# Kernel optimization log

Measured on AMD Instinct MI355X. Metric: run time of the kernel, lower is better.

The kernel has to match this reference:

```python
import math
import jax, jax.numpy as jnp
import numpy as np

CROP_H = 28  # self.height
OUT_HW = 224  # final F.interpolate size


def _thetas_and_widths(boxes_np, H, W):
    """Host-side replication of cv2.minAreaRect/getAffineTransform + param2theta.
    boxes_np: [N,1,4] int (x1,y1,x3,y3). Returns thetas [N,2,3] f32, widths [N] int."""
    thetas, widths = [], []
    for b in boxes_np:
        x1, y1, x3, y3 = [float(v) for v in b[0]]
        bw, bh = abs(x3 - x1), abs(y3 - y1)
        box_w, box_h = max(bw, bh), min(bw, bh)  # minAreaRect + swap so box_w >= box_h
        wb = min(math.ceil(CROP_H * box_w / box_h), W)
        # cv2.getAffineTransform: affine maps (x1,y1)->(0,0), (x3,y1)->(wb,0), (x1,y3)->(0,CROP_H)
        src = np.array([[x1, y1, 1.0], [x3, y1, 1.0], [x1, y3, 1.0]], dtype=np.float64)
        dst = np.array([[0.0, 0.0], [wb, 0.0], [0.0, CROP_H]], dtype=np.float64)
        P = np.linalg.solve(src, dst)           # src @ P = dst -> affine = P.T (2x3)
        A = np.vstack([P.T, [0.0, 0.0, 1.0]])   # homogeneous 3x3
        Ai = np.linalg.inv(A)                    # param2theta inverts the affine
        th = np.zeros((2, 3), dtype=np.float64)
        th[0, 0] = Ai[0, 0]
        th[0, 1] = Ai[0, 1] * H / W
        th[0, 2] = Ai[0, 2] * 2.0 / W + th[0, 0] + th[0, 1] - 1.0
        th[1, 0] = Ai[1, 0] * W / H
        th[1, 1] = Ai[1, 1]
        th[1, 2] = Ai[1, 2] * 2.0 / H + th[1, 0] + th[1, 1] - 1.0
        thetas.append(th)
        widths.append(wb)
    return np.stack(thetas).astype(np.float32), np.array(widths, dtype=np.int64)


def _interp_matrix(out_size, in_size):
    """Row-stochastic linear-interpolation matrix, bilinear align_corners=True."""
    pos = jnp.linspace(0.0, in_size - 1.0, out_size)
    i0 = jnp.clip(jnp.floor(pos), 0, in_size - 2).astype(jnp.int32)
    t = pos - i0.astype(pos.dtype)
    r = jnp.arange(out_size)
    M = jnp.zeros((out_size, in_size), jnp.float32)
    return M.at[r, i0].add(1.0 - t).at[r, i0 + 1].add(t)


def _forward(feature, boxes, num_boxes):
    C, H, W = feature.shape[1], feature.shape[2], feature.shape[3]
    boxes_np = np.asarray(boxes)
    thetas_np, widths = _thetas_and_widths(boxes_np, H, W)
    thetas = jnp.asarray(thetas_np)                              # [N,2,3]

    # F.affine_grid(theta, (N,C,H,W), align_corners=True)
    xs = jnp.linspace(-1.0, 1.0, W)
    ys = jnp.linspace(-1.0, 1.0, H)
    gx0, gy0 = jnp.meshgrid(xs, ys, indexing='xy')               # [H,W]
    base = jnp.stack([gx0, gy0, jnp.ones_like(gx0)], axis=-1)    # [H,W,3]
    grid = jnp.einsum('nij,hwj->nhwi', thetas, base)             # [N,H,W,2] (x,y)

    # F.grid_sample bilinear, padding_mode='zeros', align_corners=True
    feat0 = feature[0]                                           # [C,H,W]
    ix = (grid[..., 0] + 1.0) * (W - 1) * 0.5                    # [N,H,W]
    iy = (grid[..., 1] + 1.0) * (H - 1) * 0.5
    x0f, y0f = jnp.floor(ix), jnp.floor(iy)
    x0, y0 = x0f.astype(jnp.int32), y0f.astype(jnp.int32)
    wx, wy = ix - x0f, iy - y0f

    def g(xi, yi):
        valid = (xi >= 0) & (xi < W) & (yi >= 0) & (yi < H)
        v = feat0[:, jnp.clip(yi, 0, H - 1), jnp.clip(xi, 0, W - 1)]  # [C,N,H,W]
        return v * valid[None].astype(feat0.dtype)

    rot = (((1 - wx) * (1 - wy))[None] * g(x0, y0)
           + (wx * (1 - wy))[None] * g(x0 + 1, y0)
           + ((1 - wx) * wy)[None] * g(x0, y0 + 1)
           + (wx * wy)[None] * g(x0 + 1, y0 + 1))                 # [C,N,H,W]
    rot = jnp.transpose(rot, (1, 0, 2, 3))                        # [N,C,H,W]

    # crop [:, :, :28, :w_i] and zero-pad to max width (mask == crop+pad)
    maxw = int(widths.max())
    mask = (jnp.arange(maxw)[None, :] < jnp.asarray(widths)[:, None]).astype(rot.dtype)
    cropped = rot[:, :, :CROP_H, :maxw] * mask[:, None, None, :]  # [N,C,28,maxw]

    # sort by width descending (np.argsort then reversed, as in the original)
    order = np.argsort(widths)[::-1].copy()
    cropped = cropped[jnp.asarray(order)]

    # F.interpolate to (224,224), bilinear, align_corners=True (separable)
    My = _interp_matrix(OUT_HW, CROP_H)                           # [224,28]
    Mx = _interp_matrix(OUT_HW, maxw)                             # [224,maxw]
    return jnp.einsum('nchw,ph,qw->ncpq', cropped, My, Mx)


def setup_inputs() -> dict:
    key = jax.random.key(0)
    N, C, H, W = 32, 32, 256, 256
    feature = jax.random.normal(key, (1, C, H, W), dtype=jnp.float32)
    rng = np.random.default_rng(0)
    x1 = rng.integers(0, 170, N)
    y1 = rng.integers(0, 200, N)
    bw = rng.integers(20, 80, N)
    bh = rng.integers(8, 48, N)
    x3 = np.minimum(x1 + bw, W - 1)
    y3 = np.minimum(y1 + bh, H - 1)
    boxes = jnp.asarray(np.stack([x1, y1, x3, y3], axis=1)[:, None, :].astype(np.int64))
    return {"feature": feature, "boxes": boxes, "num_boxes": N}


def reference(feature, boxes, num_boxes):
    return _forward(feature, boxes, num_boxes)
```

## Files before the change

### kernel.cpp

```cpp
#include <hip/hip_runtime.h>

#define NBOX   32
#define NCH    32
#define IMG    256
#define CROPH  28
#define OUTHW  224
#define TSTR   257

__device__ __forceinline__ void xss_stage(long long* k, int* a,
                                          const int* p, int mask) {
  long long nk[8]; int na[8];
  for (int j = 0; j < 8; ++j) {
    long long kb = k[p[j]]; int ab = a[p[j]];
    long long mn = (kb < k[j]) ? kb : k[j];
    long long mx = (kb < k[j]) ? k[j] : kb;
    long long sel = ((mask >> j) & 1) ? mx : mn;
    na[j] = (sel == k[j]) ? a[j] : ab;
    nk[j] = sel;
  }
  for (int j = 0; j < 8; ++j) { k[j] = nk[j]; a[j] = na[j]; }
}
__device__ __forceinline__ void xss_rev(long long* k, int* a) {
  for (int j = 0; j < 4; ++j) {
    long long tk = k[j]; k[j] = k[7-j]; k[7-j] = tk;
    int ta = a[j]; a[j] = a[7-j]; a[7-j] = ta;
  }
}
__device__ __forceinline__ void xss_coex(long long* k1, int* a1,
                                         long long* k2, int* a2) {
  for (int j = 0; j < 8; ++j) {
    long long ka = k1[j], kb = k2[j];
    int aa = a1[j], ab = a2[j];
    bool alem = (ka <= kb);
    k1[j] = alem ? ka : kb;  a1[j] = alem ? aa : ab;
    k2[j] = alem ? kb : ka;  a2[j] = alem ? ab : aa;
  }
}
__device__ __forceinline__ void xss_sort8(long long* k, int* a) {
  const int P1[8] = {1,0,3,2,5,4,7,6};
  const int P2[8] = {2,3,0,1,6,7,4,5};
  const int P3[8] = {3,2,1,0,7,6,5,4};
  const int P7[8] = {7,6,5,4,3,2,1,0};
  xss_stage(k, a, P1, 0xAA);
  xss_stage(k, a, P3, 0xCC);
  xss_stage(k, a, P1, 0xAA);
  xss_stage(k, a, P7, 0xF0);
  xss_stage(k, a, P2, 0xCC);
  xss_stage(k, a, P1, 0xAA);
}
__device__ __forceinline__ void xss_merge8(long long* k, int* a) {
  const int P1[8] = {1,0,3,2,5,4,7,6};
  const int P2[8] = {2,3,0,1,6,7,4,5};
  const int P4[8] = {4,5,6,7,0,1,2,3};
  xss_stage(k, a, P4, 0xF0);
  xss_stage(k, a, P2, 0xCC);
  xss_stage(k, a, P1, 0xAA);
}
__device__ __forceinline__ void xss_merge_pair(long long* kA, int* aA,
                                               long long* kB, int* aB) {
  xss_rev(kB, aB);
  xss_coex(kA, aA, kB, aB);
  xss_rev(kB, aB);
  xss_merge8(kA, aA);
  xss_merge8(kB, aB);
}

__global__ void prep_kernel(const int* __restrict__ boxes_raw,
                            int* __restrict__ wsi, float* __restrict__ th) {
  __shared__ int    s_w[NBOX];
  __shared__ double s_t[NBOX][4];
  __shared__ int    s_asc[NBOX];
  __shared__ int    s_i64;
  int lane = threadIdx.x;

  if (lane == 0) {
    int i64 = 1;
    for (int i = 1; i < NBOX*4; i += 2)
      if (boxes_raw[i] != 0) { i64 = 0; break; }
    s_i64 = i64;
  }
  __syncthreads();
  bool i64mode = (s_i64 != 0);

  if (lane < NBOX) {
    int x1, y1, x3, y3;
    if (i64mode) {
      x1 = boxes_raw[(lane*4+0)*2]; y1 = boxes_raw[(lane*4+1)*2];
      x3 = boxes_raw[(lane*4+2)*2]; y3 = boxes_raw[(lane*4+3)*2];
    } else {
      x1 = boxes_raw[lane*4+0]; y1 = boxes_raw[lane*4+1];
      x3 = boxes_raw[lane*4+2]; y3 = boxes_raw[lane*4+3];
    }
    int bw = x3 > x1 ? x3-x1 : x1-x3;
    int bh = y3 > y1 ? y3-y1 : y1-y3;
    int bmax = bw > bh ? bw : bh;
    int bmin = bw > bh ? bh : bw;
    if (bmin < 1) bmin = 1;
    int wb = (CROPH*bmax + bmin - 1) / bmin;
    if (wb > IMG) wb = IMG;
    s_w[lane] = wb;
    double a = (double)(x3-x1) / (double)wb;
    double e = (double)(y3-y1) / (double)CROPH;
    s_t[lane][0] = a;
    s_t[lane][1] = (double)x1 * (2.0/(double)IMG) + a - 1.0;
    s_t[lane][2] = e;
    s_t[lane][3] = (double)y1 * (2.0/(double)IMG) + e - 1.0;
  }
  __syncthreads();

  if (lane == 0) {
    long long K[4][8]; int A[4][8];
    for (int v = 0; v < 4; ++v)
      for (int j = 0; j < 8; ++j) {
        A[v][j] = 8*v + j;
        K[v][j] = (long long)s_w[8*v + j];
      }
    for (int v = 0; v < 4; ++v) xss_sort8(K[v], A[v]);
    xss_merge_pair(K[0], A[0], K[1], A[1]);
    xss_merge_pair(K[2], A[2], K[3], A[3]);
    xss_rev(K[3], A[3]); xss_coex(K[0], A[0], K[3], A[3]); xss_rev(K[3], A[3]);
    xss_rev(K[2], A[2]); xss_coex(K[1], A[1], K[2], A[2]); xss_rev(K[2], A[2]);
    xss_coex(K[0], A[0], K[1], A[1]);
    xss_coex(K[2], A[2], K[3], A[3]);
    for (int v = 0; v < 4; ++v) xss_merge8(K[v], A[v]);
    for (int v = 0; v < 4; ++v)
      for (int j = 0; j < 8; ++j) s_asc[8*v + j] = A[v][j];
    int maxw = 0;
    for (int i = 0; i < NBOX; ++i) if (s_w[i] > maxw) maxw = s_w[i];
    wsi[0] = maxw;
  }
  __syncthreads();

  if (lane < NBOX) {
    int src = s_asc[NBOX-1-lane];
    wsi[1+lane]   = s_w[src];
    th[lane*4+0]  = (float)s_t[src][0];
    th[lane*4+1]  = (float)s_t[src][1];
    th[lane*4+2]  = (float)s_t[src][2];
    th[lane*4+3]  = (float)s_t[src][3];
  }
}

__global__ __launch_bounds__(256)
void fused_kernel(const float* __restrict__ feat,
                  const int* __restrict__ wsi,
                  const float* __restrict__ th,
                  float* __restrict__ out) {
  __shared__ float tile[CROPH][TSTR];
  int c = blockIdx.x, n = blockIdx.y;
  int tid = threadIdx.x;

  int maxw  = wsi[0];
  int width = wsi[1+n];
  float t00 = th[n*4+0], t02 = th[n*4+1], t11 = th[n*4+2], t12 = th[n*4+3];

  const float* fc = feat + c*IMG*IMG;
  int w = tid;
  if (w < width) {
    float gx = -1.f + (2.f/255.f)*(float)w;
    float ix = (t00*gx + t02 + 1.f)*127.5f;
    float xf = floorf(ix);
    int   x0 = (int)xf;
    x0 = min(max(x0, 0), IMG-2);
    float wx = ix - xf;
    const float* col = fc + x0;
    for (int h = 0; h < CROPH; ++h) {
      float gy = -1.f + (2.f/255.f)*(float)h;
      float iy = (t11*gy + t12 + 1.f)*127.5f;
      float yf = floorf(iy);
      int   y0 = (int)yf;
      y0 = min(max(y0, 0), IMG-2);
      float wy = iy - yf;
      const float* r0 = col + y0*IMG;
      float a0 = r0[0],   a1 = r0[1];
      float b0 = r0[IMG], b1 = r0[IMG+1];
      float ta = a0 + wx*(a1-a0);
      float tb = b0 + wx*(b1-b0);
      tile[h][w] = ta + wy*(tb-ta);
    }
  } else {
    for (int h = 0; h < CROPH; ++h) tile[h][w] = 0.f;
  }
  __syncthreads();

  int q = tid;
  if (q < OUTHW) {
    float qx = (float)q * ((float)(maxw-1)/(float)(OUTHW-1));
    float xf = floorf(qx);
    int   xi = (int)xf; if (xi > maxw-2) xi = maxw-2;
    float tx = qx - (float)xi;

    const float pys = (float)(CROPH-1)/(float)(OUTHW-1);
    float* op = out + ((size_t)(n*NCH + c)*OUTHW)*OUTHW + q;

    int cur = -2;
    float vtop = 0.f, vbot = 0.f;
    for (int p = 0; p < OUTHW; ++p) {
      float py = (float)p * pys;
      int h0 = (int)py; if (h0 > CROPH-2) h0 = CROPH-2;
      float ty = py - (float)h0;
      if (h0 != cur) {
        if (h0 == cur+1) {
          vtop = vbot;
        } else {
          float a0 = tile[h0][xi], a1 = tile[h0][xi+1];
          vtop = a0 + tx*(a1-a0);
        }
        float b0 = tile[h0+1][xi], b1 = tile[h0+1][xi+1];
        vbot = b0 + tx*(b1-b0);
        cur = h0;
      }
      *op = vtop + ty*(vbot - vtop);
      op += OUTHW;
    }
  }
}

extern "C" void kernel_launch(void* const* d_in, const int* in_sizes, int n_in,
                              void* d_out, int out_size, void* d_ws, size_t ws_size,
                              hipStream_t stream) {
  const float* feat  = (const float*)d_in[0];
  const int*   boxes = (const int*)d_in[1];
  float* out = (float*)d_out;

  int*   wsi = (int*)d_ws;
  float* th  = (float*)((char*)d_ws + 512);

  prep_kernel<<<1, 64, 0, stream>>>(boxes, wsi, th);
  fused_kernel<<<dim3(NCH, NBOX), 256, 0, stream>>>(feat, wsi, th, out);
}
```

Measured before the change: 224.9 us.

## Vectorize output stores to float4 and split output rows across waves

Each lane of the upsampling phase now computes four adjacent output columns and writes them with a single float4 store. The four waves of the block interleave over output rows, replacing the old scheme where 224 threads each walked all 224 rows. The goal is wider, more efficient global writes and more parallelism per row in the output-bound phase. The cost is that the reuse of the previous row's interpolated value now applies only within a wave's strided rows, which adds some extra shared-memory reads.

After: 220.8 us. About the same (-1.8%).

```diff
diff --git a/kernel.cpp b/kernel.cpp
--- a/kernel.cpp
+++ b/kernel.cpp
@@ -183,35 +183,52 @@
   }
   __syncthreads();
 
-  int q = tid;
-  if (q < OUTHW) {
-    float qx = (float)q * ((float)(maxw-1)/(float)(OUTHW-1));
-    float xf = floorf(qx);
-    int   xi = (int)xf; if (xi > maxw-2) xi = maxw-2;
-    float tx = qx - (float)xi;
-
+  int wave = tid >> 6;
+  int lane = tid & 63;
+  if (lane < OUTHW/4) {
+    int qb = lane * 4;
+    const float xs = (float)(maxw-1)/(float)(OUTHW-1);
+    float tx[4]; int xi[4];
+#pragma unroll
+    for (int j = 0; j < 4; ++j) {
+      float qx = (float)(qb+j) * xs;
+      float xf = floorf(qx);
+      int x = (int)xf; if (x > maxw-2) x = maxw-2;
+      xi[j] = x; tx[j] = qx - (float)x;
+    }
     const float pys = (float)(CROPH-1)/(float)(OUTHW-1);
-    float* op = out + ((size_t)(n*NCH + c)*OUTHW)*OUTHW + q;
+    float* op = out + ((size_t)(n*NCH + c))*OUTHW*OUTHW + qb;
 
     int cur = -2;
-    float vtop = 0.f, vbot = 0.f;
-    for (int p = 0; p < OUTHW; ++p) {
+    float vtop[4], vbot[4];
+    for (int p = wave; p < OUTHW; p += 4) {
       float py = (float)p * pys;
       int h0 = (int)py; if (h0 > CROPH-2) h0 = CROPH-2;
       float ty = py - (float)h0;
       if (h0 != cur) {
         if (h0 == cur+1) {
-          vtop = vbot;
+#pragma unroll
+          for (int j = 0; j < 4; ++j) vtop[j] = vbot[j];
         } else {
-          float a0 = tile[h0][xi], a1 = tile[h0][xi+1];
-          vtop = a0 + tx*(a1-a0);
+#pragma unroll
+          for (int j = 0; j < 4; ++j) {
+            float a0 = tile[h0][xi[j]], a1 = tile[h0][xi[j]+1];
+            vtop[j] = a0 + tx[j]*(a1-a0);
+          }
         }
-        float b0 = tile[h0+1][xi], b1 = tile[h0+1][xi+1];
-        vbot = b0 + tx*(b1-b0);
+#pragma unroll
+        for (int j = 0; j < 4; ++j) {
+          float b0 = tile[h0+1][xi[j]], b1 = tile[h0+1][xi[j]+1];
+          vbot[j] = b0 + tx[j]*(b1-b0);
+        }
         cur = h0;
       }
-      *op = vtop + ty*(vbot - vtop);
-      op += OUTHW;
+      float4 o;
+      o.x = vtop[0] + ty*(vbot[0]-vtop[0]);
+      o.y = vtop[1] + ty*(vbot[1]-vtop[1]);
+      o.z = vtop[2] + ty*(vbot[2]-vtop[2]);
+      o.w = vtop[3] + ty*(vbot[3]-vtop[3]);
+      *(float4*)(op + (size_t)p*OUTHW) = o;
     }
   }
 }
```
